# Kernel optimization log

Hardware: AMD Instinct MI355X
Metric: run time of the kernel (lower is better)

Reference implementation:

```python
import jax, jax.numpy as jnp
import numpy as np

NUM_EXPERTS = 16
HIDDEN = 2048
INTERMEDIATE = 1408
TOTAL_TOKENS = 32768  # tokens pre-sorted by expert assignment


def setup_inputs() -> dict:
    key = jax.random.key(0)
    k1, k2, k3, k4 = jax.random.split(key, 4)
    x = jax.random.normal(k1, (TOTAL_TOKENS, HIDDEN), dtype=jnp.float32)
    # normal() initializer per module; scale ~N(0, 0.02) like typical kernel_init
    w_gate = jax.random.normal(k2, (NUM_EXPERTS, HIDDEN, INTERMEDIATE), dtype=jnp.float32) * 0.02
    w_up = jax.random.normal(k3, (NUM_EXPERTS, HIDDEN, INTERMEDIATE), dtype=jnp.float32) * 0.02
    w_down = jax.random.normal(k4, (NUM_EXPERTS, INTERMEDIATE, HIDDEN), dtype=jnp.float32) * 0.02
    # tokens evenly distributed over experts; sums to TOTAL_TOKENS
    group_sizes = jnp.full((NUM_EXPERTS,), TOTAL_TOKENS // NUM_EXPERTS, dtype=jnp.int32)
    return {"x": x, "w_gate": w_gate, "w_up": w_up, "w_down": w_down,
            "group_sizes": group_sizes}


def reference(x, w_gate, w_up, w_down, group_sizes):
    # Grouped (ragged) GEMMs: rows of x are grouped contiguously by expert,
    # group_sizes[e] rows use expert e's kernel. lax.ragged_dot is the
    # idiomatic grouped-GEMM primitive (no dense [T,E] masking).
    gate = jax.lax.ragged_dot(x, w_gate, group_sizes)      # [T, I]
    up = jax.lax.ragged_dot(x, w_up, group_sizes)          # [T, I]
    h = jax.nn.silu(gate) * up                             # fused SwiGLU gating
    out = jax.lax.ragged_dot(h, w_down, group_sizes)       # [T, H]
    return out
```

## Files before the change

### kernel.cpp

```cpp
#include <hip/hip_runtime.h>
#include <hip/hip_bf16.h>

#define TOKENS 32768
#define NEXP   16
#define HID    2048
#define IMD    1408
#define BM 256
#define BK 64

typedef __bf16 bf16x8 __attribute__((ext_vector_type(8)));
typedef float  f32x4  __attribute__((ext_vector_type(4)));
typedef float  f32x16 __attribute__((ext_vector_type(16)));
typedef unsigned short u16x8 __attribute__((ext_vector_type(8)));

using gptr1_t = const __attribute__((address_space(1))) void*;
using lptr3_t = __attribute__((address_space(3))) void*;

static __device__ __forceinline__ unsigned short f2bf(float f) {
  unsigned int x = __builtin_bit_cast(unsigned int, f);
  x += 0x7fffu + ((x >> 16) & 1u);
  return (unsigned short)(x >> 16);
}
static __device__ __forceinline__ float bf2f(unsigned short u) {
  unsigned int x = ((unsigned int)u) << 16;
  return __builtin_bit_cast(float, x);
}
static __device__ __forceinline__ void gload16(const void* g, void* l) {
  __builtin_amdgcn_global_load_lds((gptr1_t)g, (lptr3_t)l, 16, 0, 0);
}
static __device__ __forceinline__ void vwait0() {
  asm volatile("s_waitcnt vmcnt(0)" ::: "memory");
}
static __device__ __forceinline__ void lgkm6() {
  asm volatile("s_waitcnt lgkmcnt(6)" ::: "memory");
}
static __device__ __forceinline__ void lgkm0() {
  asm volatile("s_waitcnt lgkmcnt(0)" ::: "memory");
}
static __device__ __forceinline__ f32x4 ds128(unsigned addr) {
  f32x4 d;
  asm volatile("ds_read_b128 %0, %1" : "=&v"(d) : "v"(addr));
  return d;
}

__global__ __launch_bounds__(256)
void convert_kernel(const float* __restrict__ in, unsigned short* __restrict__ out, size_t n)
{
  size_t i = ((size_t)blockIdx.x * blockDim.x + threadIdx.x) * 8;
  if (i >= n) return;
  float4 a = *(const float4*)(in + i);
  float4 b = *(const float4*)(in + i + 4);
  u16x8 o;
  o[0] = f2bf(a.x); o[1] = f2bf(a.y); o[2] = f2bf(a.z); o[3] = f2bf(a.w);
  o[4] = f2bf(b.x); o[5] = f2bf(b.y); o[6] = f2bf(b.z); o[7] = f2bf(b.w);
  *(u16x8*)(out + i) = o;
}

__global__ __launch_bounds__(256)
void transpose_conv_kernel(const float* __restrict__ in, unsigned short* __restrict__ out,
                           int K, int N)
{
  __shared__ float tile[32][33];
  const int e = blockIdx.z;
  const float* ip = in + (size_t)e * K * N;
  unsigned short* op = out + (size_t)e * K * N;
  const int c0 = blockIdx.x * 32, r0 = blockIdx.y * 32;
  const int tx = threadIdx.x, ty = threadIdx.y;
#pragma unroll
  for (int i = 0; i < 4; ++i)
    tile[ty + 8 * i][tx] = ip[(size_t)(r0 + ty + 8 * i) * N + c0 + tx];
  __syncthreads();
#pragma unroll
  for (int i = 0; i < 4; ++i)
    op[(size_t)(c0 + ty + 8 * i) * K + r0 + tx] = f2bf(tile[tx][ty + 8 * i]);
}

template<int MODE, int K, int N>
__global__ __launch_bounds__(512, 2)
void gemm_kernel(const unsigned short* __restrict__ A,
                 const unsigned short* __restrict__ B0m,
                 const unsigned short* __restrict__ B1m,
                 unsigned short* __restrict__ Hc,
                 float* __restrict__ Cf,
                 const int* __restrict__ gs)
{
  constexpr int NRT = TOKENS / BM;
  constexpr int nt  = K / BK;

  __shared__ __align__(16) unsigned short lA[2][256 * 64];
  __shared__ __align__(16) unsigned short lB[2][256 * 64];

  const int nwg = gridDim.x;
  const int qq = nwg >> 3;
  const int wgid = (blockIdx.x & 7) * qq + (blockIdx.x >> 3);
  const int rt = wgid % NRT;
  const int ct = wgid / NRT;
  const int row0 = rt * BM;

  int e = 0;
  { int a0 = 0;
    for (int i = 0; i < NEXP; ++i) { int s = gs[i]; if (row0 < a0 + s) { e = i; break; } a0 += s; } }

  const unsigned short* Ap = A + (size_t)row0 * K;
  const unsigned short* Bg = B0m + (size_t)e * N * K;
  const unsigned short* Bu = (MODE == 0) ? (B1m + (size_t)e * N * K) : nullptr;

  const int tid  = threadIdx.x;
  const int lane = tid & 63, wave = tid >> 6;
  const int wr = wave >> 2, wc = wave & 3;
  const int l31 = lane & 31, hi = lane >> 5, l7 = lane & 7;
  const int r8 = lane >> 3;
  const int slog = ((lane & 7) ^ r8) * 8;

  const unsigned sw0 = (unsigned)(((0 + hi) ^ l7) * 16);
  const unsigned sw1 = (unsigned)(((2 + hi) ^ l7) * 16);
  const unsigned sw2 = (unsigned)(((4 + hi) ^ l7) * 16);
  const unsigned sw3 = (unsigned)(((6 + hi) ^ l7) * 16);

  const unsigned lAb = (unsigned)(unsigned long long)(const void*)&lA[0][0];
  const unsigned lBb = (unsigned)(unsigned long long)(const void*)&lB[0][0];
  const unsigned aRow = lAb + (unsigned)((wr * 128 + l31) * 128);
  const unsigned bRow = lBb + (unsigned)((wc * 64 + l31) * 128);

  f32x16 acc[4][2] = {};

  auto stage = [&](int chunk, int tt) {
    const int buf = tt & 1;
    const int k0 = tt * BK;
#pragma unroll
    for (int w = 0; w < 2; ++w) {
      if (chunk >= 2) {
        const int c = chunk - 2;
        unsigned short* ldst = &lA[buf][(c * 128 + w * 64 + wave * 8) * 64];
        const int grow = c * 128 + w * 64 + wave * 8 + r8;
        gload16(Ap + (size_t)grow * K + k0 + slog, ldst);
      } else {
        unsigned short* ldst = &lB[buf][(chunk * 128 + w * 64 + wave * 8) * 64];
        const int rem = w * 64 + wave * 8 + r8;
        const int v = chunk * 128 + rem;
        if constexpr (MODE == 0) {
          const int wcq = v >> 6, p = (v >> 5) & 1, i = v & 31;
          const unsigned short* mb = p ? Bu : Bg;
          const int gcol = ct * 128 + wcq * 32 + i;
          gload16(mb + (size_t)gcol * K + k0 + slog, ldst);
        } else {
          const int gcol = ct * 256 + v;
          gload16(Bg + (size_t)gcol * K + k0 + slog, ldst);
        }
      }
    }
  };

  auto rdA = [&](f32x4* d, unsigned sw, unsigned bufoff) {
#pragma unroll
    for (int m = 0; m < 4; ++m)
      d[m] = ds128(aRow + bufoff + (unsigned)(m * 4096) + sw);
  };
  auto rdB = [&](f32x4* d, unsigned sw, unsigned bufoff) {
    d[0] = ds128(bRow + bufoff + sw);
    d[1] = ds128(bRow + bufoff + 4096u + sw);
  };
  auto cluster = [&](const f32x4* a4, const f32x4* b2) {
    __builtin_amdgcn_sched_barrier(0);
    __builtin_amdgcn_s_setprio(1);
#pragma unroll
    for (int m = 0; m < 4; ++m)
#pragma unroll
      for (int n2 = 0; n2 < 2; ++n2)
        acc[m][n2] = __builtin_amdgcn_mfma_f32_32x32x16_bf16(
            __builtin_bit_cast(bf16x8, a4[m]), __builtin_bit_cast(bf16x8, b2[n2]),
            acc[m][n2], 0, 0, 0);
    __builtin_amdgcn_s_setprio(0);
    __builtin_amdgcn_sched_barrier(0);
  };

  stage(0, 0); stage(1, 0); stage(2, 0); stage(3, 0);
  vwait0();
  __builtin_amdgcn_s_barrier();

  f32x4 aS0[4], bS0[2], aS1[4], bS1[2], aS2[4], bS2[2];

  for (int t = 0; t < nt; ++t) {
    const unsigned bufoff = (unsigned)((t & 1) * 32768);
    const bool more = (t + 1 < nt);

    rdA(aS0, sw0, bufoff); rdB(bS0, sw0, bufoff);
    rdA(aS1, sw1, bufoff); rdB(bS1, sw1, bufoff);
    lgkm6();
    cluster(aS0, bS0);
    if (more) { stage(0, t + 1); stage(1, t + 1); }
    rdA(aS2, sw2, bufoff); rdB(bS2, sw2, bufoff);
    lgkm6();
    cluster(aS1, bS1);
    if (more) { stage(2, t + 1); stage(3, t + 1); }
    rdA(aS0, sw3, bufoff); rdB(bS0, sw3, bufoff);
    lgkm6();
    cluster(aS2, bS2);
    lgkm0();
    cluster(aS0, bS0);

    vwait0();
    __builtin_amdgcn_s_barrier();
  }

#pragma unroll
  for (int m = 0; m < 4; ++m) {
    const int rowb = row0 + wr * 128 + m * 32 + 4 * hi;
    if constexpr (MODE == 0) {
      const int col = ct * 128 + wc * 32 + l31;
      f32x16 g = acc[m][0], u = acc[m][1];
#pragma unroll
      for (int r = 0; r < 16; ++r) {
        const int row = rowb + (r & 3) + 8 * (r >> 2);
        float gv = g[r];
        float s = gv / (1.f + __expf(-gv)) * u[r];
        Hc[(size_t)row * N + col] = f2bf(s);
      }
    } else {
#pragma unroll
      for (int n2 = 0; n2 < 2; ++n2) {
        const int col = ct * 256 + wc * 64 + n2 * 32 + l31;
        f32x16 v = acc[m][n2];
#pragma unroll
        for (int r = 0; r < 16; ++r) {
          const int row = rowb + (r & 3) + 8 * (r >> 2);
          Cf[(size_t)row * N + col] = v[r];
        }
      }
    }
  }
}

extern "C" void kernel_launch(void* const* d_in, const int* in_sizes, int n_in,
                              void* d_out, int out_size, void* d_ws, size_t ws_size,
                              hipStream_t stream)
{
  const float* x  = (const float*)d_in[0];
  const float* wg = (const float*)d_in[1];
  const float* wu = (const float*)d_in[2];
  const float* wd = (const float*)d_in[3];
  const int*   gs = (const int*)d_in[4];
  float* out = (float*)d_out;

  const size_t SZ_XB = (size_t)TOKENS * HID * 2;
  const size_t SZ_W  = (size_t)NEXP * HID * IMD * 2;
  const size_t SZ_H  = (size_t)TOKENS * IMD * 2;
  if (ws_size < SZ_XB + 2 * SZ_W + SZ_H) return;

  char* ws = (char*)d_ws;
  unsigned short* xb  = (unsigned short*)ws;
  unsigned short* wTg = (unsigned short*)(ws + SZ_XB);
  unsigned short* wTu = (unsigned short*)(ws + SZ_XB + SZ_W);
  unsigned short* h   = (unsigned short*)(ws + SZ_XB + 2 * SZ_W);

  const int cvt_grid = (int)(((size_t)TOKENS * HID) / (256 * 8));
  convert_kernel<<<cvt_grid, 256, 0, stream>>>(x, xb, (size_t)TOKENS * HID);

  transpose_conv_kernel<<<dim3(IMD / 32, HID / 32, NEXP), dim3(32, 8), 0, stream>>>(wg, wTg, HID, IMD);
  transpose_conv_kernel<<<dim3(IMD / 32, HID / 32, NEXP), dim3(32, 8), 0, stream>>>(wu, wTu, HID, IMD);
  gemm_kernel<0, HID, IMD><<<(TOKENS / BM) * (IMD / 128), 512, 0, stream>>>(
      xb, wTg, wTu, h, nullptr, gs);

  transpose_conv_kernel<<<dim3(HID / 32, IMD / 32, NEXP), dim3(32, 8), 0, stream>>>(wd, wTg, IMD, HID);
  gemm_kernel<1, IMD, HID><<<(TOKENS / BM) * (HID / 256), 512, 0, stream>>>(
      h, wTg, nullptr, nullptr, out, gs);
}
```

Before: 876.1 us.

## Load B operand directly from global into registers, dropping B LDS staging

Removes the LDS buffer for the weight (B) tile. Each lane now loads its MFMA B fragments straight from global memory into registers, while A is still staged through double-buffered LDS. This halves LDS footprint and LDS read traffic, which could allow higher occupancy. The cost is that B rows are no longer shared across waves with the same column group, so global and L2 traffic for B rises. The register loads are also exposed to global latency, and the plain loads are not covered by the explicit vmcnt waits.

```diff
diff --git a/kernel.cpp b/kernel.cpp
--- a/kernel.cpp
+++ b/kernel.cpp
@@ -21,18 +21,14 @@
   x += 0x7fffu + ((x >> 16) & 1u);
   return (unsigned short)(x >> 16);
 }
-static __device__ __forceinline__ float bf2f(unsigned short u) {
-  unsigned int x = ((unsigned int)u) << 16;
-  return __builtin_bit_cast(float, x);
-}
 static __device__ __forceinline__ void gload16(const void* g, void* l) {
   __builtin_amdgcn_global_load_lds((gptr1_t)g, (lptr3_t)l, 16, 0, 0);
 }
 static __device__ __forceinline__ void vwait0() {
   asm volatile("s_waitcnt vmcnt(0)" ::: "memory");
 }
-static __device__ __forceinline__ void lgkm6() {
-  asm volatile("s_waitcnt lgkmcnt(6)" ::: "memory");
+static __device__ __forceinline__ void lgkm4() {
+  asm volatile("s_waitcnt lgkmcnt(4)" ::: "memory");
 }
 static __device__ __forceinline__ void lgkm0() {
   asm volatile("s_waitcnt lgkmcnt(0)" ::: "memory");
@@ -88,7 +84,6 @@
   constexpr int nt  = K / BK;
 
   __shared__ __align__(16) unsigned short lA[2][256 * 64];
-  __shared__ __align__(16) unsigned short lB[2][256 * 64];
 
   const int nwg = gridDim.x;
   const int qq = nwg >> 3;
@@ -118,37 +113,32 @@
   const unsigned sw3 = (unsigned)(((6 + hi) ^ l7) * 16);
 
   const unsigned lAb = (unsigned)(unsigned long long)(const void*)&lA[0][0];
-  const unsigned lBb = (unsigned)(unsigned long long)(const void*)&lB[0][0];
   const unsigned aRow = lAb + (unsigned)((wr * 128 + l31) * 128);
-  const unsigned bRow = lBb + (unsigned)((wc * 64 + l31) * 128);
+
+  const unsigned short* bP0;
+  const unsigned short* bP1;
+  if constexpr (MODE == 0) {
+    const int col = ct * 128 + wc * 32 + l31;
+    bP0 = Bg + (size_t)col * K + hi * 8;
+    bP1 = Bu + (size_t)col * K + hi * 8;
+  } else {
+    bP0 = Bg + (size_t)(ct * 256 + wc * 64 + l31) * K + hi * 8;
+    bP1 = bP0 + (size_t)32 * K;
+  }
 
   f32x16 acc[4][2] = {};
 
-  auto stage = [&](int chunk, int tt) {
+  auto stageA = [&](int tt) {
     const int buf = tt & 1;
     const int k0 = tt * BK;
 #pragma unroll
-    for (int w = 0; w < 2; ++w) {
-      if (chunk >= 2) {
-        const int c = chunk - 2;
+    for (int c = 0; c < 2; ++c)
+#pragma unroll
+      for (int w = 0; w < 2; ++w) {
         unsigned short* ldst = &lA[buf][(c * 128 + w * 64 + wave * 8) * 64];
         const int grow = c * 128 + w * 64 + wave * 8 + r8;
         gload16(Ap + (size_t)grow * K + k0 + slog, ldst);
-      } else {
-        unsigned short* ldst = &lB[buf][(chunk * 128 + w * 64 + wave * 8) * 64];
-        const int rem = w * 64 + wave * 8 + r8;
-        const int v = chunk * 128 + rem;
-        if constexpr (MODE == 0) {
-          const int wcq = v >> 6, p = (v >> 5) & 1, i = v & 31;
-          const unsigned short* mb = p ? Bu : Bg;
-          const int gcol = ct * 128 + wcq * 32 + i;
-          gload16(mb + (size_t)gcol * K + k0 + slog, ldst);
-        } else {
-          const int gcol = ct * 256 + v;
-          gload16(Bg + (size_t)gcol * K + k0 + slog, ldst);
-        }
       }
-    }
   };
 
   auto rdA = [&](f32x4* d, unsigned sw, unsigned bufoff) {
@@ -156,51 +146,61 @@
     for (int m = 0; m < 4; ++m)
       d[m] = ds128(aRow + bufoff + (unsigned)(m * 4096) + sw);
   };
-  auto rdB = [&](f32x4* d, unsigned sw, unsigned bufoff) {
-    d[0] = ds128(bRow + bufoff + sw);
-    d[1] = ds128(bRow + bufoff + 4096u + sw);
-  };
-  auto cluster = [&](const f32x4* a4, const f32x4* b2) {
+  auto cluster = [&](const f32x4* a4, f32x4 bgv, f32x4 buv) {
     __builtin_amdgcn_sched_barrier(0);
     __builtin_amdgcn_s_setprio(1);
 #pragma unroll
-    for (int m = 0; m < 4; ++m)
-#pragma unroll
-      for (int n2 = 0; n2 < 2; ++n2)
-        acc[m][n2] = __builtin_amdgcn_mfma_f32_32x32x16_bf16(
-            __builtin_bit_cast(bf16x8, a4[m]), __builtin_bit_cast(bf16x8, b2[n2]),
-            acc[m][n2], 0, 0, 0);
+    for (int m = 0; m < 4; ++m) {
+      acc[m][0] = __builtin_amdgcn_mfma_f32_32x32x16_bf16(
+          __builtin_bit_cast(bf16x8, a4[m]), __builtin_bit_cast(bf16x8, bgv),
+          acc[m][0], 0, 0, 0);
+      acc[m][1] = __builtin_amdgcn_mfma_f32_32x32x16_bf16(
+          __builtin_bit_cast(bf16x8, a4[m]), __builtin_bit_cast(bf16x8, buv),
+          acc[m][1], 0, 0, 0);
+    }
     __builtin_amdgcn_s_setprio(0);
     __builtin_amdgcn_sched_barrier(0);
   };
 
-  stage(0, 0); stage(1, 0); stage(2, 0); stage(3, 0);
+  stageA(0);
   vwait0();
   __builtin_amdgcn_s_barrier();
 
-  f32x4 aS0[4], bS0[2], aS1[4], bS1[2], aS2[4], bS2[2];
-
+  f32x4 aS0[4], aS1[4], aS2[4];
+
+#pragma unroll 1
   for (int t = 0; t < nt; ++t) {
     const unsigned bufoff = (unsigned)((t & 1) * 32768);
     const bool more = (t + 1 < nt);
-
-    rdA(aS0, sw0, bufoff); rdB(bS0, sw0, bufoff);
-    rdA(aS1, sw1, bufoff); rdB(bS1, sw1, bufoff);
-    lgkm6();
-    cluster(aS0, bS0);
-    if (more) { stage(0, t + 1); stage(1, t + 1); }
-    rdA(aS2, sw2, bufoff); rdB(bS2, sw2, bufoff);
-    lgkm6();
-    cluster(aS1, bS1);
-    if (more) { stage(2, t + 1); stage(3, t + 1); }
-    rdA(aS0, sw3, bufoff); rdB(bS0, sw3, bufoff);
-    lgkm6();
-    cluster(aS2, bS2);
+    const int bo = t * 64;
+
+    f32x4 bg0 = *(const f32x4*)(bP0 + bo);
+    f32x4 bu0 = *(const f32x4*)(bP1 + bo);
+    f32x4 bg1 = *(const f32x4*)(bP0 + bo + 16);
+    f32x4 bu1 = *(const f32x4*)(bP1 + bo + 16);
+    if (more) stageA(t + 1);
+
+    rdA(aS0, sw0, bufoff);
+    rdA(aS1, sw1, bufoff);
+    lgkm4();
+    cluster(aS0, bg0, bu0);
+    f32x4 bg2 = *(const f32x4*)(bP0 + bo + 32);
+    f32x4 bu2 = *(const f32x4*)(bP1 + bo + 32);
+    f32x4 bg3 = *(const f32x4*)(bP0 + bo + 48);
+    f32x4 bu3 = *(const f32x4*)(bP1 + bo + 48);
+    rdA(aS2, sw2, bufoff);
+    lgkm4();
+    cluster(aS1, bg1, bu1);
+    rdA(aS0, sw3, bufoff);
+    lgkm4();
+    cluster(aS2, bg2, bu2);
     lgkm0();
-    cluster(aS0, bS0);
-
-    vwait0();
-    __builtin_amdgcn_s_barrier();
+    cluster(aS0, bg3, bu3);
+
+    if (more) {
+      vwait0();
+      __builtin_amdgcn_s_barrier();
+    }
   }
 
 #pragma unroll
```

Measured after the change: 1.181 ms. 34.8% more time.
